# Performance work log

Hardware: AMD Instinct MI355X
Metric: run time of the kernel (lower is better)

## Reference

```python
import jax, jax.numpy as jnp
from jax import lax
import numpy as np

# ---- init hyperparameters (from init_kwargs) ----
STRIDE = 1
DP_CHANNELS = 1
ATOM_R = 8
ATOM_C = 8
NUMB_ATOM = 128
T_SC = 3
K = 256
BATCH = 32
IMG = 64


def setup_inputs() -> dict:
    key = jax.random.key(0)
    k1, k2 = jax.random.split(key)
    Y = jax.random.normal(k1, (BATCH, DP_CHANNELS, IMG, IMG), dtype=jnp.float32)
    # ConvTranspose2d weight layout: (numb_atom, dp_channels, atom_c, atom_r)
    W = jax.random.normal(k2, (NUMB_ATOM, DP_CHANNELS, ATOM_C, ATOM_R), dtype=jnp.float32)
    # normalise_weights(): each (i, j) filter divided by its L2 norm
    W = W / jnp.sqrt(jnp.sum(W ** 2, axis=(2, 3), keepdims=True))
    return {"Y": Y, "W_D": W}


def _conv_D(X, W):
    # PyTorch ConvTranspose2d (stride=1, no padding): full convolution with
    # spatially-flipped kernel; W is (in=numb_atom, out=dp_channels, kh, kw).
    kh, kw = W.shape[2], W.shape[3]
    return lax.conv_general_dilated(
        X, jnp.flip(W, (2, 3)), (1, 1),
        [(kh - 1, kh - 1), (kw - 1, kw - 1)],
        dimension_numbers=('NCHW', 'IOHW', 'NCHW'))


def _conv_Dt(R, Wt):
    # PyTorch Conv2d (VALID, stride=1): Wt is (out=numb_atom, in=dp, kh, kw)
    return lax.conv_general_dilated(
        R, Wt, (1, 1), 'VALID', dimension_numbers=('NCHW', 'OIHW', 'NCHW'))


def _hard_threshold_k(X, k):
    # keep the k largest-|.| entries per sample (over flattened C,H,W)
    B = X.shape[0]
    flat = X.reshape(B, -1)
    _, idx = lax.top_k(jnp.abs(flat), k)                      # [B, k]
    vals = jnp.take_along_axis(flat, idx, axis=1)             # [B, k]
    out = jnp.zeros_like(flat).at[jnp.arange(B)[:, None], idx].set(vals)
    return out.reshape(X.shape)


def _linesearch(Y, X, W, Wt, k):
    R = Y - _conv_D(X, W)
    g = _conv_Dt(R, Wt)
    l2_start = jnp.sum(R ** 2)

    def attempt(alpha):
        Xu = _hard_threshold_k(X + alpha * g, k)
        err = jnp.sum((Y - _conv_D(Xu, W)) ** 2)
        return Xu, err

    Xu0, err0 = attempt(jnp.float32(1.0))

    def cond(s):
        _, _, err, count = s
        return (err >= l2_start) & (count <= 15)

    def body(s):
        alpha, _, _, count = s
        alpha = alpha * jnp.float32(0.5)
        Xu, err = attempt(alpha)
        return (alpha, Xu, err, count + 1)

    alpha, Xu, err, _ = lax.while_loop(
        cond, body, (jnp.float32(1.0), Xu0, err0, jnp.int32(0)))
    return Xu, err, alpha


def reference(Y, W_D):
    # D_trans.weight = D.weight.permute(0,1,3,2) -> (numb_atom, dp, atom_r, atom_c)
    Wt = jnp.swapaxes(W_D, 2, 3)
    kh, kw = Wt.shape[2], Wt.shape[3]
    B, _, H, W_sp = Y.shape
    X = jnp.zeros((B, W_D.shape[0], H - kh + 1, W_sp - kw + 1), dtype=Y.dtype)
    for _ in range(T_SC):
        X, _, _ = _linesearch(Y, X, W_D, Wt, K)
    return X
```

## Files before the change

### kernel.cpp

```cpp
#include <hip/hip_runtime.h>
#include <stdint.h>

#define NB   32
#define NCH  128
#define IMG  64
#define IMG2 4096
#define OH   57
#define OHW  3249
#define CHW  415872
#define KTOP 256
#define NATT 17
#define NS   32
#define SCAP 512
#define NCAP 1536
#define NBUCK 8192
#define HSHIFT 18
#define TGT  512
#define RSTRIDE 72
#define NZB  257
#define BMW  12996

typedef unsigned long long ull;

__global__ void k_init(int* support_cnt) {
    if (threadIdx.x < NB) support_cnt[threadIdx.x] = 0;
}

__global__ __launch_bounds__(256) void k_resid(
    const float* __restrict__ Y, const float* __restrict__ W,
    const double* __restrict__ l2prev, const double* __restrict__ errv,
    const uint32_t* __restrict__ sel_idx, const float* __restrict__ sel_val, int t,
    int* __restrict__ support_cnt, ull* __restrict__ sup_iv,
    float* __restrict__ Rg, double* __restrict__ l2cur,
    uint32_t* __restrict__ hist, int* __restrict__ cand_cnt)
{
    int bx = blockIdx.x, tid = threadIdx.x;
    if (bx >= NB) {
        int zb = bx - NB;
        if (zb < 256) {
            ((uint4*)hist)[zb * 256 + tid] = make_uint4(0u, 0u, 0u, 0u);
        } else {
            ((uint4*)cand_cnt)[tid] = make_uint4(0u, 0u, 0u, 0u);
        }
        return;
    }
    int b = bx;
    __shared__ float Rs[IMG2];
    __shared__ uint32_t s_si[KTOP];
    __shared__ float s_sv[KTOP];
    __shared__ double red[256];
    __shared__ int a_sh;

    const float4* Y4 = (const float4*)(Y + b * IMG2);
    float4* R4 = (float4*)Rs;
    for (int i = tid; i < IMG2 / 4; i += 256) R4[i] = Y4[i];

    int n = 0;
    if (t > 0) {
        if (tid < NATT) {
            double e = 0.0;
#pragma unroll 8
            for (int b2 = 0; b2 < NB; ++b2) e += errv[tid * NB + b2];
            red[tid] = e;
        } else if (tid == NATT) {
            double l2 = 0.0;
#pragma unroll 8
            for (int b2 = 0; b2 < NB; ++b2) l2 += l2prev[b2];
            red[NATT] = l2;
        }
        __syncthreads();
        if (tid == 0) {
            double l2 = red[NATT];
            int sel = NATT - 1;
            for (int a2 = 0; a2 < NATT; ++a2) if (red[a2] < l2) { sel = a2; break; }
            a_sh = sel;
        }
        __syncthreads();
        int a = a_sh;
        size_t o = ((size_t)a * NB + b) * KTOP;
        uint32_t mi = sel_idx[o + tid];
        float mv = sel_val[o + tid];
        s_si[tid] = mi;
        s_sv[tid] = mv;
        sup_iv[b * KTOP + tid] = (ull)mi | ((ull)__float_as_uint(mv) << 32);
        if (tid == 0) support_cnt[b] = KTOP;
        n = KTOP;
    }
    __syncthreads();

    for (int task = tid; task < n * 64; task += 256) {
        int i = task >> 6, tap = task & 63, p = tap >> 3, q = tap & 7;
        uint32_t idx = s_si[i];
        float val = s_sv[i];
        int c = idx / OHW, rem = idx % OHW, s = rem / OH, tt = rem % OH;
        float w = W[c * 64 + p * 8 + q];
        atomicAdd(&Rs[(s + p) * IMG + (tt + q)], -val * w);
    }
    __syncthreads();
    double acc = 0.0;
    for (int i = tid; i < IMG2; i += 256) {
        float v = Rs[i];
        Rg[b * IMG2 + i] = v;
        acc += (double)v * (double)v;
    }
    red[tid] = acc; __syncthreads();
    for (int s2 = 128; s2 > 0; s2 >>= 1) { if (tid < s2) red[tid] += red[tid + s2]; __syncthreads(); }
    if (tid == 0) l2cur[b] = red[0];
}

__global__ __launch_bounds__(256) void k_conv(
    const float* __restrict__ Rg, const float* __restrict__ W,
    float* __restrict__ g_out, uint32_t* __restrict__ hist)
{
    int b = blockIdx.x, cg0 = blockIdx.y, tid = threadIdx.x;
    __shared__ float Rs[71 * 72];
    __shared__ uint32_t hl[NBUCK];
    for (int i = tid; i < 71 * 72; i += 256) Rs[i] = 0.f;
    for (int i = tid; i < NBUCK; i += 256) hl[i] = 0u;
    __syncthreads();
    const float4* R4 = (const float4*)(Rg + b * IMG2);
    for (int i = tid; i < 1024; i += 256) {
        int row = i >> 4, col4 = (i & 15) * 4;
        *(float4*)&Rs[row * 72 + col4] = R4[i];
    }
    __syncthreads();
    int csub = tid >> 7;
    int tile = tid & 127;
    bool active = tile < 120;
    int tr = active ? tile / 15 : 0;
    int tc = active ? tile % 15 : 0;
    int s0 = tr * 8, t0 = tc * 4;

    for (int sub = 0; sub < 4; ++sub) {
        int c = cg0 * 8 + sub * 2 + csub;
        int c_s = __builtin_amdgcn_readfirstlane(c);
        const float* Wc = W + c_s * 64;

        float acc[8][4];
#pragma unroll
        for (int r = 0; r < 8; ++r)
#pragma unroll
            for (int cc = 0; cc < 4; ++cc) acc[r][cc] = 0.f;

#pragma unroll
        for (int rho = 0; rho < 15; ++rho) {
            float rb[12];
            const float* rp = &Rs[(s0 + rho) * 72 + t0];
            *(float4*)&rb[0] = *(const float4*)rp;
            *(float4*)&rb[4] = *(const float4*)(rp + 4);
            *(float4*)&rb[8] = *(const float4*)(rp + 8);
#pragma unroll
            for (int r = 0; r < 8; ++r) {
                const int p = rho - r;
                if (p >= 0 && p < 8) {
#pragma unroll
                    for (int q = 0; q < 8; ++q) {
                        float wv = Wc[q * 8 + p];
#pragma unroll
                        for (int cc = 0; cc < 4; ++cc)
                            acc[r][cc] = fmaf(rb[cc + q], wv, acc[r][cc]);
                    }
                }
            }
        }
        if (active) {
            float* go = g_out + (size_t)(b * NCH + c) * OHW;
#pragma unroll
            for (int r = 0; r < 8; ++r) {
                int s = s0 + r;
                if (s < OH) {
#pragma unroll
                    for (int cc = 0; cc < 4; ++cc) {
                        int tcol = t0 + cc;
                        if (tcol < OH) {
                            float v = acc[r][cc];
                            go[s * OH + tcol] = v;
                            uint32_t bits = __float_as_uint(v) & 0x7fffffffu;
                            atomicAdd(&hl[bits >> HSHIFT], 1u);
                        }
                    }
                }
            }
        }
    }
    __syncthreads();
    for (int i = tid; i < NBUCK; i += 256) {
        uint32_t v = hl[i];
        if (v) atomicAdd(&hist[b * NBUCK + i], v);
    }
}

__global__ __launch_bounds__(256) void k_thresh(const uint32_t* __restrict__ hist,
                                                uint32_t* __restrict__ thr) {
    int b = blockIdx.x, tid = threadIdx.x;
    uint32_t h[32];
    uint32_t s = 0;
    const uint32_t* hb = hist + b * NBUCK + tid * 32;
#pragma unroll
    for (int k = 0; k < 32; ++k) { h[k] = hb[k]; s += h[k]; }
    __shared__ uint32_t buf[2][256];
    int cur = 0;
    buf[0][tid] = s;
    __syncthreads();
    for (int d = 1; d < 256; d <<= 1) {
        uint32_t v = buf[cur][tid];
        if (tid + d < 256) v += buf[cur][tid + d];
        buf[cur ^ 1][tid] = v;
        cur ^= 1;
        __syncthreads();
    }
    uint32_t sufme = buf[cur][tid];
    uint32_t base  = (tid < 255) ? buf[cur][tid + 1] : 0u;
    if (tid == 0 && buf[cur][0] < TGT) thr[b] = 0u;
    if (base < TGT && sufme >= TGT) {
        uint32_t acc = base; int bk = 0;
#pragma unroll
        for (int k = 31; k >= 0; --k) {
            acc += h[k];
            if (acc >= TGT) { bk = tid * 32 + k; break; }
        }
        thr[b] = (uint32_t)bk << HSHIFT;
    }
}

__global__ __launch_bounds__(256) void k_collect(
    const float* __restrict__ g, const uint32_t* __restrict__ thr,
    int* __restrict__ cand_cnt, uint32_t* __restrict__ cand_idx, float* __restrict__ cand_g)
{
    int b = blockIdx.y;
    int i4 = blockIdx.x * 256 + threadIdx.x;
    if (i4 >= CHW / 4) return;
    int slice = blockIdx.x & (NS - 1);
    uint32_t tb = thr[b];
    float4 v4 = ((const float4*)(g + (size_t)b * CHW))[i4];
    float vv[4] = { v4.x, v4.y, v4.z, v4.w };
#pragma unroll
    for (int k = 0; k < 4; ++k) {
        uint32_t bits = __float_as_uint(vv[k]) & 0x7fffffffu;
        if (bits >= tb) {
            int pos = atomicAdd(&cand_cnt[b * NS + slice], 1);
            if (pos < SCAP) {
                cand_idx[(b * NS + slice) * SCAP + pos] = (uint32_t)(i4 * 4 + k);
                cand_g[(b * NS + slice) * SCAP + pos] = vv[k];
            }
        }
    }
}

__global__ __launch_bounds__(1024) void k_suppg(
    const float* __restrict__ g,
    const int* __restrict__ support_cnt, const ull* __restrict__ sup_iv,
    const int* __restrict__ cand_cnt, const uint32_t* __restrict__ cand_idx,
    const float* __restrict__ cand_g,
    uint4* __restrict__ ns_pack, ull* __restrict__ sup_gp, ull* __restrict__ kb_all)
{
    int b = blockIdx.x, tid = threadIdx.x, lane = tid & 63;
    __shared__ uint32_t bm[BMW];
    __shared__ int cnts[NS];
    __shared__ ull ck[NCAP];
    __shared__ float cg_l[NCAP];
    __shared__ int nns_sh;
    int n = support_cnt[b];
    for (int i = tid; i < BMW / 4; i += 1024) ((uint4*)bm)[i] = make_uint4(0u, 0u, 0u, 0u);
    if (tid < NS) cnts[tid] = min(cand_cnt[b * NS + tid], SCAP);
    if (tid == 0) nns_sh = 0;
    __syncthreads();
    if (tid < KTOP) {
        float gv = 0.f, vs = 0.f;
        uint32_t nidx;
        if (tid < n) {
            ull iv = sup_iv[b * KTOP + tid];
            uint32_t idx = (uint32_t)iv;
            nidx = idx;
            vs = __uint_as_float((uint32_t)(iv >> 32));
            atomicOr(&bm[idx >> 5], 1u << (idx & 31));
            gv = g[(size_t)b * CHW + idx];
            int c = idx / OHW, r = idx % OHW, s = r / OH, t = r % OH;
            uint32_t pk = (uint32_t)((c << 12) | (s << 6) | t);
            sup_gp[b * KTOP + tid] = ((ull)__float_as_uint(gv) << 32) | (ull)pk;
        } else {
            nidx = (uint32_t)(CHW + tid);
            sup_gp[b * KTOP + tid] = 0ull;
        }
        ull klo = (ull)(uint32_t)(~nidx);
#pragma unroll
        for (int a2 = 0; a2 < NATT; ++a2) {
            float v2 = (tid < n) ? fmaf(ldexpf(1.f, -a2), gv, vs) : 0.f;
            kb_all[((size_t)a2 * NB + b) * KTOP + tid] =
                ((ull)(__float_as_uint(v2) & 0x7fffffffu) << 32) | klo;
        }
    }
    __syncthreads();
    for (int t0 = tid; t0 < NS * SCAP; t0 += 1024) {
        int s = t0 >> 9, j = t0 & (SCAP - 1);
        bool keep = false; uint32_t idx = 0; float gv = 0.f;
        if (j < cnts[s]) {
            idx = cand_idx[(b * NS + s) * SCAP + j];
            gv = cand_g[(b * NS + s) * SCAP + j];
            keep = ((bm[idx >> 5] >> (idx & 31)) & 1u) == 0u;
        }
        ull mk = __ballot(keep);
        if (mk) {
            int basep = 0;
            if (lane == 0) basep = atomicAdd(&nns_sh, (int)__popcll(mk));
            basep = __shfl(basep, 0, 64);
            if (keep) {
                int p = basep + (int)__popcll(mk & ((1ull << lane) - 1ull));
                if (p < NCAP) {
                    ck[p] = ((ull)(__float_as_uint(gv) & 0x7fffffffu) << 32) | (ull)(uint32_t)(~idx);
                    cg_l[p] = gv;
                }
            }
        }
    }
    __syncthreads();
    int nns = min(nns_sh, NCAP);
    int nns8 = (nns + 7) & ~7;
    for (int i = nns + tid; i < nns8; i += 1024) ck[i] = 0ull;
    __syncthreads();
    ull myk[2]; int myr[2];
#pragma unroll
    for (int q = 0; q < 2; ++q) { int i = tid + 1024 * q; myk[q] = (i < nns) ? ck[i] : 0ull; myr[q] = 0; }
    for (int j = 0; j < nns8; j += 8) {
        ull t0 = ck[j], t1 = ck[j+1], t2 = ck[j+2], t3 = ck[j+3];
        ull t4 = ck[j+4], t5 = ck[j+5], t6 = ck[j+6], t7 = ck[j+7];
#pragma unroll
        for (int q = 0; q < 2; ++q) {
            myr[q] += ((t0 > myk[q]) ? 1 : 0) + ((t1 > myk[q]) ? 1 : 0)
                    + ((t2 > myk[q]) ? 1 : 0) + ((t3 > myk[q]) ? 1 : 0)
                    + ((t4 > myk[q]) ? 1 : 0) + ((t5 > myk[q]) ? 1 : 0)
                    + ((t6 > myk[q]) ? 1 : 0) + ((t7 > myk[q]) ? 1 : 0);
        }
    }
#pragma unroll
    for (int q = 0; q < 2; ++q) {
        int i = tid + 1024 * q;
        if (i < nns && myr[q] < KTOP) {
            uint32_t idx = ~(uint32_t)myk[q];
            int r = myr[q];
            int c = idx / OHW, rr = idx % OHW, s = rr / OH, t = rr % OH;
            uint32_t pk = (uint32_t)((c << 12) | (s << 6) | t);
            ns_pack[b * KTOP + r] = make_uint4(idx, __float_as_uint(cg_l[i]), pk, 0u);
        }
    }
}

__global__ __launch_bounds__(512) void k_att2(
    const float* __restrict__ Y, const float* __restrict__ W,
    const int* __restrict__ support_cnt, const ull* __restrict__ sup_iv,
    const ull* __restrict__ sup_gp, const uint4* __restrict__ ns_pack,
    const ull* __restrict__ kb_all,
    uint32_t* __restrict__ sel_idx, float* __restrict__ sel_val, double* __restrict__ err,
    float* __restrict__ outz, int zf)
{
    int a = blockIdx.x, b = blockIdx.y, tid = threadIdx.x;
    int lane = tid & 63, wid = tid >> 6;
    float alpha = ldexpf(1.f, -a);
    int n = support_cnt[b];

    __shared__ float recon[64 * RSTRIDE];
    __shared__ ull kA[KTOP];
    __shared__ ull s_pv[KTOP];
    __shared__ uint32_t s_idx[KTOP];
    __shared__ double redd[8];

    uint32_t myi = 0, mypk = 0;
    float myv = 0.f;
    ull myk = 0;
    if (tid < KTOP) {
        uint4 np = ns_pack[b * KTOP + tid];
        myi = np.x;
        myv = alpha * __uint_as_float(np.y);
        mypk = np.z;
        myk = ((ull)(__float_as_uint(myv) & 0x7fffffffu) << 32) | (ull)(uint32_t)(~myi);
        kA[tid] = myk;
    } else {
        int t2 = tid - KTOP;
        ull gp = sup_gp[b * KTOP + t2];
        ull iv = sup_iv[b * KTOP + t2];
        if (t2 < n) {
            myi = (uint32_t)iv;
            myv = fmaf(alpha, __uint_as_float((uint32_t)(gp >> 32)),
                       __uint_as_float((uint32_t)(iv >> 32)));
            mypk = (uint32_t)gp;
        } else {
            myi = (uint32_t)(CHW + t2);
            myv = 0.f; mypk = 0u;
        }
        myk = ((ull)(__float_as_uint(myv) & 0x7fffffffu) << 32) | (ull)(uint32_t)(~myi);
    }

    const float4* Y4 = (const float4*)(Y + b * IMG2);
    float4 y0 = Y4[tid * 2], y1 = Y4[tid * 2 + 1];

    for (int i = tid; i < 64 * RSTRIDE; i += 512) recon[i] = 0.f;
    __syncthreads();

    const ull* __restrict__ kb = kb_all + ((size_t)a * NB + b) * KTOP;
    int cb0 = 0, cb1 = 0;
    for (int j = 0; j < KTOP; j += 8) {
        ull t0 = kb[j],     t1 = kb[j + 1], t2 = kb[j + 2], t3 = kb[j + 3];
        ull t4 = kb[j + 4], t5 = kb[j + 5], t6 = kb[j + 6], t7 = kb[j + 7];
        cb0 += ((t0 > myk) ? 1 : 0) + ((t1 > myk) ? 1 : 0)
             + ((t2 > myk) ? 1 : 0) + ((t3 > myk) ? 1 : 0);
        cb1 += ((t4 > myk) ? 1 : 0) + ((t5 > myk) ? 1 : 0)
             + ((t6 > myk) ? 1 : 0) + ((t7 > myk) ? 1 : 0);
    }
    int cb = cb0 + cb1;
    int rank;
    if (tid < KTOP) {
        rank = tid + cb;
    } else {
        int lo = 0, hi = KTOP;
        while (lo < hi) { int mid = (lo + hi) >> 1; if (kA[mid] > myk) lo = mid + 1; else hi = mid; }
        rank = lo + cb;
    }
    if (rank < KTOP) {
        s_pv[rank] = ((ull)__float_as_uint(myv) << 32) | (ull)mypk;
        s_idx[rank] = myi;
    }
    __syncthreads();

    {
        int p = lane >> 3, q = lane & 7;
        ull pv[4]; float wv[4];
#pragma unroll
        for (int j = 0; j < 4; ++j) pv[j] = s_pv[wid + 8 * j];
#pragma unroll
        for (int j = 0; j < 4; ++j) wv[j] = W[(((uint32_t)pv[j]) >> 12) * 64 + lane];
#pragma unroll
        for (int k4 = 0; k4 < 32; k4 += 4) {
            ull npv[4] = {0, 0, 0, 0}; float nwv[4] = {0.f, 0.f, 0.f, 0.f};
            if (k4 + 4 < 32) {
#pragma unroll
                for (int j = 0; j < 4; ++j) npv[j] = s_pv[wid + 8 * (k4 + 4 + j)];
#pragma unroll
                for (int j = 0; j < 4; ++j) nwv[j] = W[(((uint32_t)npv[j]) >> 12) * 64 + lane];
            }
#pragma unroll
            for (int j = 0; j < 4; ++j) {
                uint32_t pk = (uint32_t)pv[j];
                float val = __uint_as_float((uint32_t)(pv[j] >> 32));
                int s = (pk >> 6) & 63, t = pk & 63;
                atomicAdd(&recon[(s + p) * RSTRIDE + (t + q)], val * wv[j]);
            }
#pragma unroll
            for (int j = 0; j < 4; ++j) { pv[j] = npv[j]; wv[j] = nwv[j]; }
        }
    }
    __syncthreads();

    double accd = 0.0;
    {
        int idx0 = tid * 2;
        const float* rr = &recon[(idx0 >> 4) * RSTRIDE + (idx0 & 15) * 4];
        float d0 = y0.x - rr[0]; accd += (double)d0 * (double)d0;
        float d1 = y0.y - rr[1]; accd += (double)d1 * (double)d1;
        float d2 = y0.z - rr[2]; accd += (double)d2 * (double)d2;
        float d3 = y0.w - rr[3]; accd += (double)d3 * (double)d3;
        int idx1 = tid * 2 + 1;
        rr = &recon[(idx1 >> 4) * RSTRIDE + (idx1 & 15) * 4];
        float e0 = y1.x - rr[0]; accd += (double)e0 * (double)e0;
        float e1 = y1.y - rr[1]; accd += (double)e1 * (double)e1;
        float e2 = y1.z - rr[2]; accd += (double)e2 * (double)e2;
        float e3 = y1.w - rr[3]; accd += (double)e3 * (double)e3;
    }
    for (int d = 32; d > 0; d >>= 1) accd += __shfl_xor(accd, d, 64);
    if (lane == 0) redd[wid] = accd;
    __syncthreads();
    if (tid == 0) {
        double e = 0.0;
#pragma unroll
        for (int w2 = 0; w2 < 8; ++w2) e += redd[w2];
        err[a * NB + b] = e;
    }

    if (tid < KTOP) {
        size_t o = ((size_t)a * NB + b) * KTOP;
        ull pvt = s_pv[tid];
        sel_idx[o + tid] = s_idx[tid];
        sel_val[o + tid] = __uint_as_float((uint32_t)(pvt >> 32));
    }

    if (zf) {
        float4* o4 = (float4*)outz;
        size_t fb = (size_t)a * NB + b;
        for (size_t i = fb * 512 + tid; i < (size_t)NB * CHW / 4; i += (size_t)NATT * NB * 512)
            o4[i] = make_float4(0.f, 0.f, 0.f, 0.f);
    }
}

__global__ __launch_bounds__(256) void k_scatter2(
    const double* __restrict__ l2f, const double* __restrict__ errv,
    const uint32_t* __restrict__ sel_idx, const float* __restrict__ sel_val,
    float* __restrict__ out)
{
    int b = blockIdx.x, tid = threadIdx.x;
    __shared__ double red2[NATT + 1];
    __shared__ int a_sh;
    if (tid < NATT) {
        double e = 0.0;
#pragma unroll 8
        for (int b2 = 0; b2 < NB; ++b2) e += errv[tid * NB + b2];
        red2[tid] = e;
    } else if (tid == NATT) {
        double l2 = 0.0;
#pragma unroll 8
        for (int b2 = 0; b2 < NB; ++b2) l2 += l2f[b2];
        red2[NATT] = l2;
    }
    __syncthreads();
    if (tid == 0) {
        double l2 = red2[NATT];
        int sel = NATT - 1;
        for (int a2 = 0; a2 < NATT; ++a2) if (red2[a2] < l2) { sel = a2; break; }
        a_sh = sel;
    }
    __syncthreads();
    size_t o = ((size_t)a_sh * NB + b) * KTOP;
    out[(size_t)b * CHW + sel_idx[o + tid]] = sel_val[o + tid];
}

static size_t align256(size_t x) { return (x + 255) & ~(size_t)255; }

extern "C" void kernel_launch(void* const* d_in, const int* in_sizes, int n_in,
                              void* d_out, int out_size, void* d_ws, size_t ws_size,
                              hipStream_t stream)
{
    const float* Y = (const float*)d_in[0];
    const float* W = (const float*)d_in[1];
    float* out = (float*)d_out;

    char* p = (char*)d_ws;
    size_t off = 0;
    auto carve = [&](size_t bytes) { void* r = p + off; off = align256(off + bytes); return r; };
    float*    Rg          = (float*)   carve(NB * IMG2 * sizeof(float));
    uint32_t* hist        = (uint32_t*)carve((size_t)NB * NBUCK * sizeof(uint32_t));
    uint32_t* thr         = (uint32_t*)carve(NB * sizeof(uint32_t));
    int*      cand_cnt    = (int*)     carve(NB * NS * sizeof(int));
    double*   l2part      = (double*)  carve(2 * NB * sizeof(double));
    double*   err         = (double*)  carve((size_t)NATT * NB * sizeof(double));
    int*      support_cnt = (int*)     carve(NB * sizeof(int));
    ull*      sup_iv      = (ull*)     carve((size_t)NB * KTOP * sizeof(ull));
    uint32_t* sel_idx     = (uint32_t*)carve((size_t)NATT * NB * KTOP * sizeof(uint32_t));
    float*    sel_val     = (float*)   carve((size_t)NATT * NB * KTOP * sizeof(float));
    uint32_t* cand_idx    = (uint32_t*)carve((size_t)NB * NS * SCAP * sizeof(uint32_t));
    float*    cand_g      = (float*)   carve((size_t)NB * NS * SCAP * sizeof(float));
    uint4*    ns_pack     = (uint4*)   carve((size_t)NB * KTOP * sizeof(uint4));
    ull*      sup_gp      = (ull*)     carve((size_t)NB * KTOP * sizeof(ull));
    ull*      kb_all      = (ull*)     carve((size_t)NATT * NB * KTOP * sizeof(ull));
    (void)ws_size; (void)in_sizes; (void)n_in; (void)out_size;

    k_init<<<1, 64, 0, stream>>>(support_cnt);
    for (int t = 0; t < 3; ++t) {
        double* l2cur  = l2part + (t & 1) * NB;
        double* l2prev = l2part + ((t + 1) & 1) * NB;
        k_resid<<<NB + NZB, 256, 0, stream>>>(Y, W, l2prev, err, sel_idx, sel_val, t,
                                              support_cnt, sup_iv, Rg, l2cur, hist, cand_cnt);
        k_conv<<<dim3(NB, 16), 256, 0, stream>>>(Rg, W, out, hist);
        k_thresh<<<NB, 256, 0, stream>>>(hist, thr);
        k_collect<<<dim3((CHW / 4 + 255) / 256, NB), 256, 0, stream>>>(out, thr, cand_cnt, cand_idx, cand_g);
        k_suppg<<<NB, 1024, 0, stream>>>(out, support_cnt, sup_iv,
                                         cand_cnt, cand_idx, cand_g,
                                         ns_pack, sup_gp, kb_all);
        k_att2<<<dim3(NATT, NB), 512, 0, stream>>>(Y, W, support_cnt, sup_iv,
                                                   sup_gp, ns_pack, kb_all,
                                                   sel_idx, sel_val, err,
                                                   out, (t == 2) ? 1 : 0);
    }
    k_scatter2<<<NB, 256, 0, stream>>>(l2part, err, sel_idx, sel_val, out);
}
```

Baseline: 642.4 us.

## Fuse residual computation into conv kernel and move buffer zeroing into consumers

Removes the separate residual kernel. Each of the 16 channel-group blocks per sample now rebuilds the residual Y - D*X directly in its padded shared tile and computes the L2 norm there, instead of writing and re-reading a global residual buffer. Histogram and candidate-counter zeroing moves into k_init and into the tail of the threshold and support kernels, which saves one launch per iteration. In exchange, the sparse scatter of 256x64 atomic adds is repeated in all 16 blocks per sample.

```diff
diff --git a/kernel.cpp b/kernel.cpp
--- a/kernel.cpp
+++ b/kernel.cpp
@@ -17,43 +17,41 @@
 #define HSHIFT 18
 #define TGT  512
 #define RSTRIDE 72
-#define NZB  257
 #define BMW  12996
 
 typedef unsigned long long ull;
 
-__global__ void k_init(int* support_cnt) {
-    if (threadIdx.x < NB) support_cnt[threadIdx.x] = 0;
-}
-
-__global__ __launch_bounds__(256) void k_resid(
+__global__ __launch_bounds__(256) void k_init(
+    uint32_t* __restrict__ hist, int* __restrict__ cand_cnt, int* __restrict__ support_cnt)
+{
+    int bx = blockIdx.x, tid = threadIdx.x;
+    if (bx < 256) {
+        ((uint4*)hist)[bx * 256 + tid] = make_uint4(0u, 0u, 0u, 0u);
+    } else {
+        ((uint4*)cand_cnt)[tid] = make_uint4(0u, 0u, 0u, 0u);
+        if (tid < NB) support_cnt[tid] = 0;
+    }
+}
+
+__global__ __launch_bounds__(256) void k_conv2(
     const float* __restrict__ Y, const float* __restrict__ W,
     const double* __restrict__ l2prev, const double* __restrict__ errv,
     const uint32_t* __restrict__ sel_idx, const float* __restrict__ sel_val, int t,
     int* __restrict__ support_cnt, ull* __restrict__ sup_iv,
-    float* __restrict__ Rg, double* __restrict__ l2cur,
-    uint32_t* __restrict__ hist, int* __restrict__ cand_cnt)
-{
-    int bx = blockIdx.x, tid = threadIdx.x;
-    if (bx >= NB) {
-        int zb = bx - NB;
-        if (zb < 256) {
-            ((uint4*)hist)[zb * 256 + tid] = make_uint4(0u, 0u, 0u, 0u);
-        } else {
-            ((uint4*)cand_cnt)[tid] = make_uint4(0u, 0u, 0u, 0u);
-        }
-        return;
-    }
-    int b = bx;
-    __shared__ float Rs[IMG2];
+    float* __restrict__ g_out, uint32_t* __restrict__ hist,
+    double* __restrict__ l2cur)
+{
+    int b = blockIdx.x, cg0 = blockIdx.y, tid = threadIdx.x;
+    int lane = tid & 63, wid = tid >> 6;
+    __shared__ float Rs[71 * 72];
+    __shared__ uint32_t hl[NBUCK];
+    __shared__ double redl2[256];
     __shared__ uint32_t s_si[KTOP];
     __shared__ float s_sv[KTOP];
-    __shared__ double red[256];
     __shared__ int a_sh;
 
-    const float4* Y4 = (const float4*)(Y + b * IMG2);
-    float4* R4 = (float4*)Rs;
-    for (int i = tid; i < IMG2 / 4; i += 256) R4[i] = Y4[i];
+    for (int i = tid; i < 71 * 72; i += 256) Rs[i] = 0.f;
+    for (int i = tid; i < NBUCK; i += 256) hl[i] = 0u;
 
     int n = 0;
     if (t > 0) {
@@ -61,18 +59,18 @@
             double e = 0.0;
 #pragma unroll 8
             for (int b2 = 0; b2 < NB; ++b2) e += errv[tid * NB + b2];
-            red[tid] = e;
+            redl2[tid] = e;
         } else if (tid == NATT) {
             double l2 = 0.0;
 #pragma unroll 8
             for (int b2 = 0; b2 < NB; ++b2) l2 += l2prev[b2];
-            red[NATT] = l2;
+            redl2[NATT] = l2;
         }
         __syncthreads();
         if (tid == 0) {
-            double l2 = red[NATT];
+            double l2 = redl2[NATT];
             int sel = NATT - 1;
-            for (int a2 = 0; a2 < NATT; ++a2) if (red[a2] < l2) { sel = a2; break; }
+            for (int a2 = 0; a2 < NATT; ++a2) if (redl2[a2] < l2) { sel = a2; break; }
             a_sh = sel;
         }
         __syncthreads();
@@ -82,9 +80,18 @@
         float mv = sel_val[o + tid];
         s_si[tid] = mi;
         s_sv[tid] = mv;
-        sup_iv[b * KTOP + tid] = (ull)mi | ((ull)__float_as_uint(mv) << 32);
-        if (tid == 0) support_cnt[b] = KTOP;
+        if (cg0 == 0) {
+            sup_iv[b * KTOP + tid] = (ull)mi | ((ull)__float_as_uint(mv) << 32);
+            if (tid == 0) support_cnt[b] = KTOP;
+        }
         n = KTOP;
+    }
+    __syncthreads();
+
+    const float4* Y4 = (const float4*)(Y + b * IMG2);
+    for (int i = tid; i < 1024; i += 256) {
+        int row = i >> 4, col4 = (i & 15) * 4;
+        *(float4*)&Rs[row * 72 + col4] = Y4[i];
     }
     __syncthreads();
 
@@ -94,36 +101,19 @@
         float val = s_sv[i];
         int c = idx / OHW, rem = idx % OHW, s = rem / OH, tt = rem % OH;
         float w = W[c * 64 + p * 8 + q];
-        atomicAdd(&Rs[(s + p) * IMG + (tt + q)], -val * w);
-    }
-    __syncthreads();
-    double acc = 0.0;
-    for (int i = tid; i < IMG2; i += 256) {
-        float v = Rs[i];
-        Rg[b * IMG2 + i] = v;
-        acc += (double)v * (double)v;
-    }
-    red[tid] = acc; __syncthreads();
-    for (int s2 = 128; s2 > 0; s2 >>= 1) { if (tid < s2) red[tid] += red[tid + s2]; __syncthreads(); }
-    if (tid == 0) l2cur[b] = red[0];
-}
-
-__global__ __launch_bounds__(256) void k_conv(
-    const float* __restrict__ Rg, const float* __restrict__ W,
-    float* __restrict__ g_out, uint32_t* __restrict__ hist)
-{
-    int b = blockIdx.x, cg0 = blockIdx.y, tid = threadIdx.x;
-    __shared__ float Rs[71 * 72];
-    __shared__ uint32_t hl[NBUCK];
-    for (int i = tid; i < 71 * 72; i += 256) Rs[i] = 0.f;
-    for (int i = tid; i < NBUCK; i += 256) hl[i] = 0u;
-    __syncthreads();
-    const float4* R4 = (const float4*)(Rg + b * IMG2);
-    for (int i = tid; i < 1024; i += 256) {
-        int row = i >> 4, col4 = (i & 15) * 4;
-        *(float4*)&Rs[row * 72 + col4] = R4[i];
-    }
-    __syncthreads();
+        atomicAdd(&Rs[(s + p) * 72 + (tt + q)], -val * w);
+    }
+    __syncthreads();
+
+    {
+        double acc = 0.0;
+        for (int i = tid; i < 71 * 72; i += 256) { float v = Rs[i]; acc += (double)v * (double)v; }
+        for (int d = 32; d > 0; d >>= 1) acc += __shfl_xor(acc, d, 64);
+        if (lane == 0) redl2[wid] = acc;
+        __syncthreads();
+        if (cg0 == 0 && tid == 0) l2cur[b] = redl2[0] + redl2[1] + redl2[2] + redl2[3];
+    }
+
     int csub = tid >> 7;
     int tile = tid & 127;
     bool active = tile < 120;
@@ -190,8 +180,8 @@
     }
 }
 
-__global__ __launch_bounds__(256) void k_thresh(const uint32_t* __restrict__ hist,
-                                                uint32_t* __restrict__ thr) {
+__global__ __launch_bounds__(256) void k_thresh2(uint32_t* __restrict__ hist,
+                                                 uint32_t* __restrict__ thr) {
     int b = blockIdx.x, tid = threadIdx.x;
     uint32_t h[32];
     uint32_t s = 0;
@@ -221,6 +211,9 @@
         }
         thr[b] = (uint32_t)bk << HSHIFT;
     }
+    __syncthreads();
+    for (int i = tid; i < NBUCK / 4; i += 256)
+        ((uint4*)(hist + (size_t)b * NBUCK))[i] = make_uint4(0u, 0u, 0u, 0u);
 }
 
 __global__ __launch_bounds__(256) void k_collect(
@@ -247,10 +240,10 @@
     }
 }
 
-__global__ __launch_bounds__(1024) void k_suppg(
+__global__ __launch_bounds__(1024) void k_suppg2(
     const float* __restrict__ g,
     const int* __restrict__ support_cnt, const ull* __restrict__ sup_iv,
-    const int* __restrict__ cand_cnt, const uint32_t* __restrict__ cand_idx,
+    int* __restrict__ cand_cnt, const uint32_t* __restrict__ cand_idx,
     const float* __restrict__ cand_g,
     uint4* __restrict__ ns_pack, ull* __restrict__ sup_gp, ull* __restrict__ kb_all)
 {
@@ -343,6 +336,7 @@
             ns_pack[b * KTOP + r] = make_uint4(idx, __float_as_uint(cg_l[i]), pk, 0u);
         }
     }
+    if (tid < NS) cand_cnt[b * NS + tid] = 0;
 }
 
 __global__ __launch_bounds__(512) void k_att2(
@@ -534,7 +528,6 @@
     char* p = (char*)d_ws;
     size_t off = 0;
     auto carve = [&](size_t bytes) { void* r = p + off; off = align256(off + bytes); return r; };
-    float*    Rg          = (float*)   carve(NB * IMG2 * sizeof(float));
     uint32_t* hist        = (uint32_t*)carve((size_t)NB * NBUCK * sizeof(uint32_t));
     uint32_t* thr         = (uint32_t*)carve(NB * sizeof(uint32_t));
     int*      cand_cnt    = (int*)     carve(NB * NS * sizeof(int));
@@ -551,18 +544,17 @@
     ull*      kb_all      = (ull*)     carve((size_t)NATT * NB * KTOP * sizeof(ull));
     (void)ws_size; (void)in_sizes; (void)n_in; (void)out_size;
 
-    k_init<<<1, 64, 0, stream>>>(support_cnt);
+    k_init<<<257, 256, 0, stream>>>(hist, cand_cnt, support_cnt);
     for (int t = 0; t < 3; ++t) {
         double* l2cur  = l2part + (t & 1) * NB;
         double* l2prev = l2part + ((t + 1) & 1) * NB;
-        k_resid<<<NB + NZB, 256, 0, stream>>>(Y, W, l2prev, err, sel_idx, sel_val, t,
-                                              support_cnt, sup_iv, Rg, l2cur, hist, cand_cnt);
-        k_conv<<<dim3(NB, 16), 256, 0, stream>>>(Rg, W, out, hist);
-        k_thresh<<<NB, 256, 0, stream>>>(hist, thr);
+        k_conv2<<<dim3(NB, 16), 256, 0, stream>>>(Y, W, l2prev, err, sel_idx, sel_val, t,
+                                                  support_cnt, sup_iv, out, hist, l2cur);
+        k_thresh2<<<NB, 256, 0, stream>>>(hist, thr);
         k_collect<<<dim3((CHW / 4 + 255) / 256, NB), 256, 0, stream>>>(out, thr, cand_cnt, cand_idx, cand_g);
-        k_suppg<<<NB, 1024, 0, stream>>>(out, support_cnt, sup_iv,
-                                         cand_cnt, cand_idx, cand_g,
-                                         ns_pack, sup_gp, kb_all);
+        k_suppg2<<<NB, 1024, 0, stream>>>(out, support_cnt, sup_iv,
+                                          cand_cnt, cand_idx, cand_g,
+                                          ns_pack, sup_gp, kb_all);
         k_att2<<<dim3(NATT, NB), 512, 0, stream>>>(Y, W, support_cnt, sup_iv,
                                                    sup_gp, ns_pack, kb_all,
                                                    sel_idx, sel_val, err,
```

New measurement: 681.3 us. 1.06x slower.
